# Optimization experiments

Measured on AMD Instinct MI355X. Metric: run time of the kernel, lower is better.

## Reference

```python
import jax, jax.numpy as jnp
import numpy as np

B, C, H, W = 2048, 16, 32, 32
F = C * H * W  # 16384, flattened feature dim
NAN_FRAC = 0.1


def setup_inputs() -> dict:
    key = jax.random.key(0)
    k1, k2, k3, k4, k5, k6 = jax.random.split(key, 6)
    output = jax.random.normal(k1, (B, C, H, W), dtype=jnp.float32)
    target = jax.random.normal(k2, (B, C, H, W), dtype=jnp.float32)
    # inject NaNs so the nan-omission path is exercised
    nan_mask = jax.random.uniform(k6, (B, C, H, W)) < NAN_FRAC
    target = jnp.where(nan_mask, jnp.nan, target)
    e_exp = jax.random.uniform(k3, (B, 1), dtype=jnp.float32)
    sample_weight = jax.random.uniform(k4, (B, 1), dtype=jnp.float32)
    feature_weight = jax.random.uniform(k5, (F, 1), dtype=jnp.float32)
    return {"output": output, "target": target, "e_exp": e_exp,
            "sample_weight": sample_weight, "feature_weight": feature_weight}


def reference(output, target, e_exp, sample_weight, feature_weight):
    # NaN-omitted, feature-weighted, per-sample-normalized MSE.
    # (e_exp and sample_weight are accepted but unused, as in the original.)
    num_pos = ~jnp.isnan(target)                       # [B,C,H,W] bool
    tgt = jnp.where(num_pos, target, 0.0)
    maskf = num_pos.astype(output.dtype)
    residual = (tgt - output) * maskf                  # [B,C,H,W]
    residual = residual.reshape(residual.shape[0], -1)  # [B,F]
    # torch.mm(residual, diag(fw)) == residual * fw^T (elementwise, same math)
    standardized = residual * feature_weight[:, 0][None, :]  # [B,F]
    per_sample = jnp.sum(standardized ** 2, axis=1) / jnp.sum(
        maskf.reshape(maskf.shape[0], -1), axis=1)     # [B]
    return jnp.sum(per_sample)
```

## Files before the change

kernel.cpp:

```cpp
#include <hip/hip_runtime.h>
#include <math.h>


#define B_SAMPLES 2048
#define F_FEATURES 16384
#define THREADS 256
#define CHUNKS 4
#define F_CHUNK (F_FEATURES / CHUNKS)
#define V_PER_THREAD (F_CHUNK / 4 / THREADS)

typedef float fx4 __attribute__((ext_vector_type(4)));

__device__ __forceinline__ void accum(const fx4 t, const fx4 o, const fx4 w,
                                      float& sumsq, float& cnt) {
    #pragma unroll
    for (int j = 0; j < 4; ++j) {
        const bool m = !isnan(t[j]);
        const float r = m ? (t[j] - o[j]) * w[j] : 0.0f;
        sumsq = fmaf(r, r, sumsq);
        cnt += m ? 1.0f : 0.0f;
    }
}

__global__ __launch_bounds__(THREADS) void fnmse_partial(
    const float* __restrict__ output,
    const float* __restrict__ target,
    const float* __restrict__ fw,
    float* __restrict__ ws_sq,
    float* __restrict__ ws_ct)
{
    const int b = blockIdx.x >> 2;
    const int c = blockIdx.x & 3;
    const int tid = threadIdx.x;

    const fx4* __restrict__ o4 = (const fx4*)(output + (size_t)b * F_FEATURES + c * F_CHUNK);
    const fx4* __restrict__ t4 = (const fx4*)(target + (size_t)b * F_FEATURES + c * F_CHUNK);
    const fx4* __restrict__ w4 = (const fx4*)(fw + c * F_CHUNK);

    float sumsq = 0.0f;
    float cnt   = 0.0f;

    fx4 o_c = __builtin_nontemporal_load(o4 + tid);
    fx4 t_c = __builtin_nontemporal_load(t4 + tid);
    fx4 w_c = w4[tid];

    #pragma unroll
    for (int k = 0; k < V_PER_THREAD; ++k) {
        fx4 o_n, t_n, w_n;
        if (k + 1 < V_PER_THREAD) {
            const int v = (k + 1) * THREADS + tid;
            o_n = __builtin_nontemporal_load(o4 + v);
            t_n = __builtin_nontemporal_load(t4 + v);
            w_n = w4[v];
        }
        accum(t_c, o_c, w_c, sumsq, cnt);
        o_c = o_n; t_c = t_n; w_c = w_n;
    }

    #pragma unroll
    for (int off = 32; off > 0; off >>= 1) {
        sumsq += __shfl_down(sumsq, off, 64);
        cnt   += __shfl_down(cnt,   off, 64);
    }

    __shared__ float s_sq[THREADS / 64];
    __shared__ float s_ct[THREADS / 64];
    const int wave = tid >> 6;
    const int lane = tid & 63;
    if (lane == 0) { s_sq[wave] = sumsq; s_ct[wave] = cnt; }
    __syncthreads();

    if (tid == 0) {
        const float sq = s_sq[0] + s_sq[1] + s_sq[2] + s_sq[3];
        const float ct = s_ct[0] + s_ct[1] + s_ct[2] + s_ct[3];
        atomicAdd(&ws_sq[b], sq);
        atomicAdd(&ws_ct[b], ct);
    }
}

__global__ __launch_bounds__(THREADS) void fnmse_finalize(
    const float* __restrict__ ws_sq,
    const float* __restrict__ ws_ct,
    float* __restrict__ out)
{
    const int tid = threadIdx.x;
    float acc = 0.0f;
    #pragma unroll
    for (int s = 0; s < B_SAMPLES / THREADS; ++s) {
        const int b = s * THREADS + tid;
        acc += ws_sq[b] / ws_ct[b];
    }
    #pragma unroll
    for (int off = 32; off > 0; off >>= 1)
        acc += __shfl_down(acc, off, 64);

    __shared__ float s_a[THREADS / 64];
    const int wave = tid >> 6;
    const int lane = tid & 63;
    if (lane == 0) s_a[wave] = acc;
    __syncthreads();
    if (tid == 0) out[0] = s_a[0] + s_a[1] + s_a[2] + s_a[3];
}

extern "C" void kernel_launch(void* const* d_in, const int* in_sizes, int n_in,
                              void* d_out, int out_size, void* d_ws, size_t ws_size,
                              hipStream_t stream) {
    const float* output = (const float*)d_in[0];
    const float* target = (const float*)d_in[1];
    const float* fw     = (const float*)d_in[4];
    float* out = (float*)d_out;

    float* ws_sq = (float*)d_ws;
    float* ws_ct = ws_sq + B_SAMPLES;

    (void)hipMemsetAsync(d_ws, 0, 2 * B_SAMPLES * sizeof(float), stream);

    fnmse_partial<<<B_SAMPLES * CHUNKS, THREADS, 0, stream>>>(output, target, fw, ws_sq, ws_ct);
    fnmse_finalize<<<1, THREADS, 0, stream>>>(ws_sq, ws_ct, out);
}
```

Before: 255.9 us.

## Issue all loads upfront and replace atomics with per-chunk partial writes

Each thread now loads all of its output and target vectors before any compute, instead of prefetching one step ahead, so more memory requests are in flight per wave. The per-sample atomicAdd is replaced by writing each block's partial sums to its own slot, and the finalize kernel sums the four chunks per sample. This removes the workspace memset launch and the atomics, at the cost of more registers per thread and a larger workspace.

```diff
diff --git a/kernel.cpp b/kernel.cpp
--- a/kernel.cpp
+++ b/kernel.cpp
@@ -10,17 +10,6 @@
 #define V_PER_THREAD (F_CHUNK / 4 / THREADS)
 
 typedef float fx4 __attribute__((ext_vector_type(4)));
-
-__device__ __forceinline__ void accum(const fx4 t, const fx4 o, const fx4 w,
-                                      float& sumsq, float& cnt) {
-    #pragma unroll
-    for (int j = 0; j < 4; ++j) {
-        const bool m = !isnan(t[j]);
-        const float r = m ? (t[j] - o[j]) * w[j] : 0.0f;
-        sumsq = fmaf(r, r, sumsq);
-        cnt += m ? 1.0f : 0.0f;
-    }
-}
 
 __global__ __launch_bounds__(THREADS) void fnmse_partial(
     const float* __restrict__ output,
@@ -37,24 +26,28 @@
     const fx4* __restrict__ t4 = (const fx4*)(target + (size_t)b * F_FEATURES + c * F_CHUNK);
     const fx4* __restrict__ w4 = (const fx4*)(fw + c * F_CHUNK);
 
+    fx4 o[V_PER_THREAD], t[V_PER_THREAD], w[V_PER_THREAD];
+    #pragma unroll
+    for (int k = 0; k < V_PER_THREAD; ++k) {
+        const int v = k * THREADS + tid;
+        o[k] = __builtin_nontemporal_load(o4 + v);
+        t[k] = __builtin_nontemporal_load(t4 + v);
+    }
+    #pragma unroll
+    for (int k = 0; k < V_PER_THREAD; ++k)
+        w[k] = w4[k * THREADS + tid];
+
     float sumsq = 0.0f;
     float cnt   = 0.0f;
-
-    fx4 o_c = __builtin_nontemporal_load(o4 + tid);
-    fx4 t_c = __builtin_nontemporal_load(t4 + tid);
-    fx4 w_c = w4[tid];
-
     #pragma unroll
     for (int k = 0; k < V_PER_THREAD; ++k) {
-        fx4 o_n, t_n, w_n;
-        if (k + 1 < V_PER_THREAD) {
-            const int v = (k + 1) * THREADS + tid;
-            o_n = __builtin_nontemporal_load(o4 + v);
-            t_n = __builtin_nontemporal_load(t4 + v);
-            w_n = w4[v];
+        #pragma unroll
+        for (int j = 0; j < 4; ++j) {
+            const bool m = !isnan(t[k][j]);
+            const float r = m ? (t[k][j] - o[k][j]) * w[k][j] : 0.0f;
+            sumsq = fmaf(r, r, sumsq);
+            cnt += m ? 1.0f : 0.0f;
         }
-        accum(t_c, o_c, w_c, sumsq, cnt);
-        o_c = o_n; t_c = t_n; w_c = w_n;
     }
 
     #pragma unroll
@@ -71,10 +64,8 @@
     __syncthreads();
 
     if (tid == 0) {
-        const float sq = s_sq[0] + s_sq[1] + s_sq[2] + s_sq[3];
-        const float ct = s_ct[0] + s_ct[1] + s_ct[2] + s_ct[3];
-        atomicAdd(&ws_sq[b], sq);
-        atomicAdd(&ws_ct[b], ct);
+        ws_sq[b * CHUNKS + c] = s_sq[0] + s_sq[1] + s_sq[2] + s_sq[3];
+        ws_ct[b * CHUNKS + c] = s_ct[0] + s_ct[1] + s_ct[2] + s_ct[3];
     }
 }
 
@@ -84,11 +75,16 @@
     float* __restrict__ out)
 {
     const int tid = threadIdx.x;
+    const fx4* __restrict__ sq4 = (const fx4*)ws_sq;
+    const fx4* __restrict__ ct4 = (const fx4*)ws_ct;
+
     float acc = 0.0f;
     #pragma unroll
     for (int s = 0; s < B_SAMPLES / THREADS; ++s) {
         const int b = s * THREADS + tid;
-        acc += ws_sq[b] / ws_ct[b];
+        const fx4 q = sq4[b];
+        const fx4 n = ct4[b];
+        acc += ((q[0] + q[1]) + (q[2] + q[3])) / ((n[0] + n[1]) + (n[2] + n[3]));
     }
     #pragma unroll
     for (int off = 32; off > 0; off >>= 1)
@@ -111,9 +107,8 @@
     float* out = (float*)d_out;
 
     float* ws_sq = (float*)d_ws;
-    float* ws_ct = ws_sq + B_SAMPLES;
+    float* ws_ct = ws_sq + B_SAMPLES * CHUNKS;
 
-    (void)hipMemsetAsync(d_ws, 0, 2 * B_SAMPLES * sizeof(float), stream);
 
     fnmse_partial<<<B_SAMPLES * CHUNKS, THREADS, 0, stream>>>(output, target, fw, ws_sq, ws_ct);
     fnmse_finalize<<<1, THREADS, 0, stream>>>(ws_sq, ws_ct, out);
```

New measurement: 250.1 us, median of 2. 1.02x faster.
